# Performance work log

Hardware: AMD Instinct MI355X
Metric: run time of the kernel (lower is better)

## Reference

```python
import jax, jax.numpy as jnp
import numpy as np

MAXDISP = 48


def setup_inputs() -> dict:
    key = jax.random.key(0)
    k1, k2 = jax.random.split(key)
    B, C, H, W = 4, 32, 64, 128
    x = jax.random.normal(k1, (B, C, H, W), dtype=jnp.float32)
    y = jax.random.normal(k2, (B, C, H, W), dtype=jnp.float32)
    return {"x": x, "y": y}


def reference(x, y):
    # cost[b, :C, d, h, w]   = x[b, :, h, w]     if w >= d else 0
    # cost[b, C:, d, h, w]   = y[b, :, h, w - d] if w >= d else 0
    B, C, H, W = x.shape
    D = MAXDISP
    d = jnp.arange(D)[:, None]            # [D, 1]
    w = jnp.arange(W)[None, :]            # [1, W]
    mask = (w >= d)                       # [D, W]
    mask_b = mask[None, None, :, None, :] # [1, 1, D, 1, W]

    # left features: broadcast over D, mask out w < d
    x_part = jnp.where(mask_b, x[:, :, None, :, :], 0.0)  # [B, C, D, H, W]

    # right features: gather shifted columns w - d (clipped), then mask
    y_idx = jnp.maximum(w - d, 0)                         # [D, W]
    y_g = jnp.take(y, y_idx, axis=3)                      # [B, C, H, D, W]
    y_g = jnp.transpose(y_g, (0, 1, 3, 2, 4))             # [B, C, D, H, W]
    y_part = jnp.where(mask_b, y_g, 0.0)

    return jnp.concatenate([x_part, y_part], axis=1)      # [B, 2C, D, H, W]
```

## Files before the change

### kernel.cpp

```cpp
#include <hip/hip_runtime.h>


#define CV_B 4
#define CV_C 32
#define CV_D 48
#define CV_H 64
#define CV_W 128
#define CV_W4 (CV_W / 4)
#define CV_TOTAL4 (CV_B * 2 * CV_C * CV_D * CV_H * CV_W4)

__global__ __launch_bounds__(256) void cost_volume_kernel(
    const float* __restrict__ x, const float* __restrict__ y,
    float4* __restrict__ out)
{
    int tid = blockIdx.x * blockDim.x + threadIdx.x;
    int idx = tid;
    const int w4 = idx & (CV_W4 - 1);
    idx >>= 5;
    const int h = idx & (CV_H - 1);
    idx >>= 6;
    const int d = idx % CV_D;
    idx /= CV_D;
    const int c = idx & 63;
    const int b = idx >> 6;

    const int w0 = w4 * 4;
    float4 v;
    if (c < CV_C) {
        const float4* xr =
            (const float4*)(x + (((b * CV_C + c) * CV_H + h) * CV_W));
        const float4 xv = xr[w4];
        v.x = (w0 + 0 >= d) ? xv.x : 0.0f;
        v.y = (w0 + 1 >= d) ? xv.y : 0.0f;
        v.z = (w0 + 2 >= d) ? xv.z : 0.0f;
        v.w = (w0 + 3 >= d) ? xv.w : 0.0f;
    } else {
        const float* yr =
            y + (((b * CV_C + (c - CV_C)) * CV_H + h) * CV_W);
        v.x = (w0 + 0 >= d) ? yr[w0 + 0 - d] : 0.0f;
        v.y = (w0 + 1 >= d) ? yr[w0 + 1 - d] : 0.0f;
        v.z = (w0 + 2 >= d) ? yr[w0 + 2 - d] : 0.0f;
        v.w = (w0 + 3 >= d) ? yr[w0 + 3 - d] : 0.0f;
    }
    out[tid] = v;
}

extern "C" void kernel_launch(void* const* d_in, const int* in_sizes, int n_in,
                              void* d_out, int out_size, void* d_ws, size_t ws_size,
                              hipStream_t stream) {
    const float* x = (const float*)d_in[0];
    const float* y = (const float*)d_in[1];
    float4* out = (float4*)d_out;

    const int block = 256;
    const int grid = CV_TOTAL4 / block;
    cost_volume_kernel<<<grid, block, 0, stream>>>(x, y, out);
}
```

Measured before the change: 444.3 us.

## Loop over disparities per thread and shift y columns with warp shuffles

Each thread now handles one (b, channel, h, w4) position and loops over all 48 disparities, loading the input once and writing 48 float4 outputs. For the y half, shifted columns come from a width-32 __shfl_up of the previous lane's float4 instead of repeated unaligned scalar global loads. This cuts redundant input reads and index math but reduces the grid 48x. Lane 0 of each 32-wide row receives its own value from the shuffle, which is harmless only because positions with w < d are masked to zero.

Result: faster. 388.6 us (-12.6%).

```diff
diff --git a/kernel.cpp b/kernel.cpp
--- a/kernel.cpp
+++ b/kernel.cpp
@@ -1,48 +1,57 @@
 #include <hip/hip_runtime.h>
 
 
-#define CV_B 4
-#define CV_C 32
-#define CV_D 48
-#define CV_H 64
-#define CV_W 128
-#define CV_W4 (CV_W / 4)
-#define CV_TOTAL4 (CV_B * 2 * CV_C * CV_D * CV_H * CV_W4)
+#define CV_DSTRIDE (64 * 32)
 
 __global__ __launch_bounds__(256) void cost_volume_kernel(
     const float* __restrict__ x, const float* __restrict__ y,
     float4* __restrict__ out)
 {
-    int tid = blockIdx.x * blockDim.x + threadIdx.x;
-    int idx = tid;
-    const int w4 = idx & (CV_W4 - 1);
-    idx >>= 5;
-    const int h = idx & (CV_H - 1);
-    idx >>= 6;
-    const int d = idx % CV_D;
-    idx /= CV_D;
-    const int c = idx & 63;
-    const int b = idx >> 6;
+    const int tid = blockIdx.x * 256 + threadIdx.x;
+    const int w4 = tid & 31;
+    const int h  = (tid >> 5) & 63;
+    const int cc = (tid >> 11) & 63;
+    const int b  = tid >> 17;
+    const int w0 = w4 * 4;
 
-    const int w0 = w4 * 4;
-    float4 v;
-    if (c < CV_C) {
-        const float4* xr =
-            (const float4*)(x + (((b * CV_C + c) * CV_H + h) * CV_W));
-        const float4 xv = xr[w4];
-        v.x = (w0 + 0 >= d) ? xv.x : 0.0f;
-        v.y = (w0 + 1 >= d) ? xv.y : 0.0f;
-        v.z = (w0 + 2 >= d) ? xv.z : 0.0f;
-        v.w = (w0 + 3 >= d) ? xv.w : 0.0f;
+    float4* outp = out + (((((b * 64 + cc) * 48) * 64 + h) * 32) + w4);
+
+#define STORE_D(dv, e0, e1, e2, e3)                        \
+    {                                                      \
+        const int d_ = (dv);                               \
+        float4 v;                                          \
+        v.x = (w0 + 0 >= d_) ? (e0) : 0.0f;                \
+        v.y = (w0 + 1 >= d_) ? (e1) : 0.0f;                \
+        v.z = (w0 + 2 >= d_) ? (e2) : 0.0f;                \
+        v.w = (w0 + 3 >= d_) ? (e3) : 0.0f;                \
+        outp[d_ * CV_DSTRIDE] = v;                         \
+    }
+
+    if (cc < 32) {
+        const float4 xv =
+            *(const float4*)(x + ((b * 32 + cc) * 64 + h) * 128 + w0);
+#pragma unroll
+        for (int d = 0; d < 48; ++d) {
+            STORE_D(d, xv.x, xv.y, xv.z, xv.w);
+        }
     } else {
-        const float* yr =
-            y + (((b * CV_C + (c - CV_C)) * CV_H + h) * CV_W);
-        v.x = (w0 + 0 >= d) ? yr[w0 + 0 - d] : 0.0f;
-        v.y = (w0 + 1 >= d) ? yr[w0 + 1 - d] : 0.0f;
-        v.z = (w0 + 2 >= d) ? yr[w0 + 2 - d] : 0.0f;
-        v.w = (w0 + 3 >= d) ? yr[w0 + 3 - d] : 0.0f;
+        float4 cur =
+            *(const float4*)(y + ((b * 32 + (cc - 32)) * 64 + h) * 128 + w0);
+#pragma unroll
+        for (int q = 0; q < 12; ++q) {
+            float4 prev;
+            prev.x = __shfl_up(cur.x, 1, 32);
+            prev.y = __shfl_up(cur.y, 1, 32);
+            prev.z = __shfl_up(cur.z, 1, 32);
+            prev.w = __shfl_up(cur.w, 1, 32);
+            STORE_D(4 * q + 0, cur.x,  cur.y,  cur.z,  cur.w);
+            STORE_D(4 * q + 1, prev.w, cur.x,  cur.y,  cur.z);
+            STORE_D(4 * q + 2, prev.z, prev.w, cur.x,  cur.y);
+            STORE_D(4 * q + 3, prev.y, prev.z, prev.w, cur.x);
+            cur = prev;
+        }
     }
-    out[tid] = v;
+#undef STORE_D
 }
 
 extern "C" void kernel_launch(void* const* d_in, const int* in_sizes, int n_in,
@@ -53,6 +62,6 @@
     float4* out = (float4*)d_out;
 
     const int block = 256;
-    const int grid = CV_TOTAL4 / block;
+    const int grid = (4 * 64 * 64 * 32) / block;
     cost_volume_kernel<<<grid, block, 0, stream>>>(x, y, out);
 }
```
